# Kernel tuning notes

Hardware: AMD Instinct MI355X
Metric: run time of the kernel (lower is better)

Reference implementation:

```python
import jax, jax.numpy as jnp
import numpy as np


def setup_inputs() -> dict:
    key = jax.random.key(0)
    x = jax.random.normal(key, (8, 32, 128, 32, 32), dtype=jnp.float32)
    return {"x": x}


def _gram_schmidt(y):
    # y: [M, C, N, D]; orthogonalize the N vectors (length D) per (M, C)
    n = y.shape[2]
    v0 = y[:, :, 0, :]
    b0 = v0 / jnp.linalg.norm(v0, axis=-1, keepdims=True)
    b0 = jnp.where(jnp.isnan(b0), 0.0, b0)  # torch sets only NaN -> 0
    basis = jnp.zeros_like(y).at[:, :, 0, :].set(b0)

    def step(basis, i):
        v = y[:, :, i, :]                                   # [M, C, D]
        # zero (unfilled) basis rows contribute nothing, so using the full
        # buffer matches the growing-basis math exactly
        coeff = jnp.einsum('mcd,mcnd->mcn', v, basis)       # v . b_j
        proj = jnp.einsum('mcn,mcnd->mcd', coeff, basis)    # sum_j (v.b_j) b_j
        w = v - proj
        wn = w / jnp.linalg.norm(w, axis=-1, keepdims=True)
        wn = jnp.where(jnp.isnan(wn), 0.0, wn)
        return basis.at[:, :, i, :].set(wn), None

    basis, _ = jax.lax.scan(step, basis, jnp.arange(1, n))
    return basis


def reference(x):
    N, M, C, H, W = x.shape
    D = H * W
    y = x.reshape(N, M, C, D).transpose(1, 2, 0, 3)  # [M, C, N, D]
    basis = _gram_schmidt(y)
    # [M, C, N, D] -> [N, M, C, D] -> [N, M, C, H, W]
    return basis.transpose(2, 0, 1, 3).reshape(N, M, C, H, W)
```

## Files before the change

### kernel.cpp

```cpp
#include <hip/hip_runtime.h>


#define MC   4096
#define DIM  1024
#define NV   8
#define TPB  128
#define E    8
#define IDX(i,j) ((i)*((i)+1)/2+(j))

typedef float f32x4 __attribute__((ext_vector_type(4)));

template <int CTRL, int ROWM>
__device__ __forceinline__ float dpp_add(float x) {
    const int m = __builtin_amdgcn_update_dpp(
        0, __float_as_int(x), CTRL, ROWM, 0xf, false);
    return x + __int_as_float(m);
}

__device__ __forceinline__ float wave_sum(float x) {
    x = dpp_add<0x111, 0xf>(x);
    x = dpp_add<0x112, 0xf>(x);
    x = dpp_add<0x114, 0xf>(x);
    x = dpp_add<0x118, 0xf>(x);
    x = dpp_add<0x142, 0xa>(x);
    x = dpp_add<0x143, 0xc>(x);
    return x;
}

__global__ __launch_bounds__(TPB) void gs_kernel(const float* __restrict__ x,
                                                 float* __restrict__ out) {
    const int mc   = blockIdx.x;
    const int t    = threadIdx.x;
    const int lane = t & 63;
    const int wave = t >> 6;

    __shared__ float red[2][36];

    const size_t strideN = (size_t)MC * DIM;
    const size_t base    = (size_t)mc * DIM;

    float v[NV][E];
#pragma unroll
    for (int n = 0; n < NV; ++n) {
        const float4 a = *reinterpret_cast<const float4*>(x + n * strideN + base + (size_t)t * 4);
        const float4 b = *reinterpret_cast<const float4*>(x + n * strideN + base + 512 + (size_t)t * 4);
        v[n][0] = a.x; v[n][1] = a.y; v[n][2] = a.z; v[n][3] = a.w;
        v[n][4] = b.x; v[n][5] = b.y; v[n][6] = b.z; v[n][7] = b.w;
    }

    float g[36];
#pragma unroll
    for (int i = 0; i < NV; ++i) {
#pragma unroll
        for (int j = 0; j <= i; ++j) {
            float s = 0.0f;
#pragma unroll
            for (int e = 0; e < E; ++e) s += v[i][e] * v[j][e];
            g[IDX(i, j)] = s;
        }
    }

#pragma unroll
    for (int k = 0; k < 36; ++k) g[k] = wave_sum(g[k]);

    if (lane == 63) {
#pragma unroll
        for (int k = 0; k < 36; ++k) red[wave][k] = g[k];
    }
    __syncthreads();
#pragma unroll
    for (int k = 0; k < 36; ++k) g[k] = red[0][k] + red[1][k];

    float rdiag[NV];
#pragma unroll
    for (int i = 0; i < NV; ++i) {
#pragma unroll
        for (int j = 0; j < i; ++j) {
            float s = g[IDX(i, j)];
#pragma unroll
            for (int p = 0; p < NV; ++p) {
                if (p >= j) break;
                s -= g[IDX(i, p)] * g[IDX(j, p)];
            }
            g[IDX(i, j)] = s * rdiag[j];
        }
        float d = g[IDX(i, i)];
#pragma unroll
        for (int p = 0; p < NV; ++p) {
            if (p >= i) break;
            d -= g[IDX(i, p)] * g[IDX(i, p)];
        }
        g[IDX(i, i)] = (d > 0.0f) ? sqrtf(d) : 0.0f;
        rdiag[i]     = (d > 0.0f) ? rsqrtf(d) : 0.0f;
    }

#pragma unroll
    for (int i = 0; i < NV; ++i) {
#pragma unroll
        for (int j = 0; j < NV; ++j) {
            if (j >= i) break;
            const float lij = g[IDX(i, j)];
#pragma unroll
            for (int e = 0; e < E; ++e) v[i][e] -= lij * v[j][e];
        }
        const float r = rdiag[i];
#pragma unroll
        for (int e = 0; e < E; ++e) v[i][e] *= r;
    }

#pragma unroll
    for (int n = 0; n < NV; ++n) {
        f32x4* p0 = reinterpret_cast<f32x4*>(out + n * strideN + base + (size_t)t * 4);
        f32x4* p1 = reinterpret_cast<f32x4*>(out + n * strideN + base + 512 + (size_t)t * 4);
        f32x4 a; a.x = v[n][0]; a.y = v[n][1]; a.z = v[n][2]; a.w = v[n][3];
        f32x4 b; b.x = v[n][4]; b.y = v[n][5]; b.z = v[n][6]; b.w = v[n][7];
        __builtin_nontemporal_store(a, p0);
        __builtin_nontemporal_store(b, p1);
    }
}

extern "C" void kernel_launch(void* const* d_in, const int* in_sizes, int n_in,
                              void* d_out, int out_size, void* d_ws, size_t ws_size,
                              hipStream_t stream) {
    const float* x = (const float*)d_in[0];
    float* out = (float*)d_out;
    gs_kernel<<<MC, TPB, 0, stream>>>(x, out);
}
```

Measured before the change: 246.6 us.

## Make blocks persistent over four slices with double-buffered register prefetch

Launches 1024 blocks of 256 threads. Each block processes four (m,c) slices in turn, prefetching the next slice's eight vectors into a second register buffer while it computes the Gram matrix, Cholesky and output for the current one. Each thread now holds four elements per vector instead of eight, and the cross-wave reduction sums four partials. The goal is to hide global load latency behind compute on this memory-bound kernel. In exchange it adds an extra __syncthreads per step and more registers for the double buffer, and it launches fewer blocks.

Result: slower. 261.1 us (+5.9%).

```diff
diff --git a/kernel.cpp b/kernel.cpp
--- a/kernel.cpp
+++ b/kernel.cpp
@@ -1,11 +1,13 @@
 #include <hip/hip_runtime.h>
 
 
-#define MC   4096
-#define DIM  1024
-#define NV   8
-#define TPB  128
-#define E    8
+#define MC    4096
+#define DIM   1024
+#define NV    8
+#define TPB   256
+#define NBLK  1024
+#define ITERS 4
+#define E     4
 #define IDX(i,j) ((i)*((i)+1)/2+(j))
 
 typedef float f32x4 __attribute__((ext_vector_type(4)));
@@ -27,49 +29,47 @@
     return x;
 }
 
-__global__ __launch_bounds__(TPB) void gs_kernel(const float* __restrict__ x,
-                                                 float* __restrict__ out) {
-    const int mc   = blockIdx.x;
-    const int t    = threadIdx.x;
-    const int lane = t & 63;
-    const int wave = t >> 6;
-
-    __shared__ float red[2][36];
-
+__device__ __forceinline__ void load_vecs(const float* __restrict__ x,
+                                          size_t base, float (&v)[NV][E]) {
     const size_t strideN = (size_t)MC * DIM;
-    const size_t base    = (size_t)mc * DIM;
-
-    float v[NV][E];
 #pragma unroll
     for (int n = 0; n < NV; ++n) {
-        const float4 a = *reinterpret_cast<const float4*>(x + n * strideN + base + (size_t)t * 4);
-        const float4 b = *reinterpret_cast<const float4*>(x + n * strideN + base + 512 + (size_t)t * 4);
-        v[n][0] = a.x; v[n][1] = a.y; v[n][2] = a.z; v[n][3] = a.w;
-        v[n][4] = b.x; v[n][5] = b.y; v[n][6] = b.z; v[n][7] = b.w;
+        const f32x4 f = *reinterpret_cast<const f32x4*>(x + n * strideN + base);
+        v[n][0] = f.x; v[n][1] = f.y; v[n][2] = f.z; v[n][3] = f.w;
     }
+}
+
+template <bool PREFETCH>
+__device__ __forceinline__ void step(const float* __restrict__ x,
+                                     float* __restrict__ out,
+                                     float (&cur)[NV][E], float (&nxt)[NV][E],
+                                     size_t cur_base, size_t nxt_base,
+                                     float (*red)[36], int lane, int wave) {
+    if (PREFETCH) load_vecs(x, nxt_base, nxt);
 
     float g[36];
 #pragma unroll
-    for (int i = 0; i < NV; ++i) {
+    for (int i = 0; i < NV; ++i)
 #pragma unroll
         for (int j = 0; j <= i; ++j) {
             float s = 0.0f;
 #pragma unroll
-            for (int e = 0; e < E; ++e) s += v[i][e] * v[j][e];
+            for (int e = 0; e < E; ++e) s += cur[i][e] * cur[j][e];
             g[IDX(i, j)] = s;
         }
-    }
 
 #pragma unroll
     for (int k = 0; k < 36; ++k) g[k] = wave_sum(g[k]);
 
+    __syncthreads();
     if (lane == 63) {
 #pragma unroll
         for (int k = 0; k < 36; ++k) red[wave][k] = g[k];
     }
     __syncthreads();
 #pragma unroll
-    for (int k = 0; k < 36; ++k) g[k] = red[0][k] + red[1][k];
+    for (int k = 0; k < 36; ++k)
+        g[k] = red[0][k] + red[1][k] + red[2][k] + red[3][k];
 
     float rdiag[NV];
 #pragma unroll
@@ -101,22 +101,41 @@
             if (j >= i) break;
             const float lij = g[IDX(i, j)];
 #pragma unroll
-            for (int e = 0; e < E; ++e) v[i][e] -= lij * v[j][e];
+            for (int e = 0; e < E; ++e) cur[i][e] -= lij * cur[j][e];
         }
         const float r = rdiag[i];
 #pragma unroll
-        for (int e = 0; e < E; ++e) v[i][e] *= r;
+        for (int e = 0; e < E; ++e) cur[i][e] *= r;
     }
 
+    const size_t strideN = (size_t)MC * DIM;
 #pragma unroll
     for (int n = 0; n < NV; ++n) {
-        f32x4* p0 = reinterpret_cast<f32x4*>(out + n * strideN + base + (size_t)t * 4);
-        f32x4* p1 = reinterpret_cast<f32x4*>(out + n * strideN + base + 512 + (size_t)t * 4);
-        f32x4 a; a.x = v[n][0]; a.y = v[n][1]; a.z = v[n][2]; a.w = v[n][3];
-        f32x4 b; b.x = v[n][4]; b.y = v[n][5]; b.z = v[n][6]; b.w = v[n][7];
-        __builtin_nontemporal_store(a, p0);
-        __builtin_nontemporal_store(b, p1);
+        f32x4 f; f.x = cur[n][0]; f.y = cur[n][1]; f.z = cur[n][2]; f.w = cur[n][3];
+        __builtin_nontemporal_store(
+            f, reinterpret_cast<f32x4*>(out + n * strideN + cur_base));
     }
+}
+
+__global__ __launch_bounds__(TPB, 4) void gs_kernel(const float* __restrict__ x,
+                                                    float* __restrict__ out) {
+    const int t    = threadIdx.x;
+    const int lane = t & 63;
+    const int wave = t >> 6;
+
+    __shared__ float red[4][36];
+
+    const size_t b0 = (size_t)(blockIdx.x + 0 * NBLK) * DIM + (size_t)t * 4;
+    const size_t b1 = (size_t)(blockIdx.x + 1 * NBLK) * DIM + (size_t)t * 4;
+    const size_t b2 = (size_t)(blockIdx.x + 2 * NBLK) * DIM + (size_t)t * 4;
+    const size_t b3 = (size_t)(blockIdx.x + 3 * NBLK) * DIM + (size_t)t * 4;
+
+    float A[NV][E], B[NV][E];
+    load_vecs(x, b0, A);
+    step<true >(x, out, A, B, b0, b1, red, lane, wave);
+    step<true >(x, out, B, A, b1, b2, red, lane, wave);
+    step<true >(x, out, A, B, b2, b3, red, lane, wave);
+    step<false>(x, out, B, A, b3, b3, red, lane, wave);
 }
 
 extern "C" void kernel_launch(void* const* d_in, const int* in_sizes, int n_in,
@@ -124,5 +143,5 @@
                               hipStream_t stream) {
     const float* x = (const float*)d_in[0];
     float* out = (float*)d_out;
-    gs_kernel<<<MC, TPB, 0, stream>>>(x, out);
+    gs_kernel<<<NBLK, TPB, 0, stream>>>(x, out);
 }
```
